# Kernel tuning notes

Hardware: AMD Instinct MI355X
Metric: run time of the kernel (lower is better)

Reference implementation:

```python
import jax, jax.numpy as jnp
import numpy as np

B, S, H, NH = 8, 4096, 1024, 16
HD = H // NH


def setup_inputs() -> dict:
    key = jax.random.key(0)
    ks = jax.random.split(key, 8)
    sd = 1.0 / np.sqrt(H)
    return {
        "hidden_states": jax.random.normal(ks[0], (B, S, H), jnp.float32),
        "attention_mask": jnp.zeros((B, 1, S), jnp.float32),
        "Wq": jax.random.normal(ks[1], (H, H), jnp.float32) * sd,
        "bq": jnp.zeros((H,), jnp.float32),
        "Wqa": jax.random.normal(ks[2], (H, NH), jnp.float32) * sd,
        "bqa": jnp.zeros((NH,), jnp.float32),
        "Wk": jax.random.normal(ks[3], (H, H), jnp.float32) * sd,
        "bk": jnp.zeros((H,), jnp.float32),
        "Wka": jax.random.normal(ks[4], (H, NH), jnp.float32) * sd,
        "bka": jnp.zeros((NH,), jnp.float32),
        "Wt": jax.random.normal(ks[5], (H, H), jnp.float32) * sd,
        "bt": jnp.zeros((H,), jnp.float32),
    }


def reference(hidden_states, attention_mask, Wq, bq, Wqa, bqa, Wk, bk, Wka, bka, Wt, bt):
    b, s, h = hidden_states.shape
    nh = Wqa.shape[1]
    hd = h // nh
    scale = 1.0 / np.sqrt(hd).astype(np.float32)

    mq = hidden_states @ Wq + bq                      # [b,s,h]
    mk = hidden_states @ Wk + bk                      # [b,s,h]

    # global query pooling
    qs = jnp.swapaxes(mq @ Wqa + bqa, 1, 2) * scale + attention_mask   # [b,nh,s]
    qw = jax.nn.softmax(qs, axis=-1)                  # [b,nh,s]
    ql = jnp.swapaxes(mq.reshape(b, s, nh, hd), 1, 2) # [b,nh,s,hd]
    pq = jnp.einsum('bns,bnsd->bnd', qw, ql).reshape(b, 1, h)  # pooled query, broadcast over seq

    # elementwise gating + global key pooling
    mqk = mk * pq                                     # [b,s,h]
    qks = jnp.swapaxes(mqk @ Wka + bka, 1, 2) * scale + attention_mask  # [b,nh,s]
    qkw = jax.nn.softmax(qks, axis=-1)                # [b,nh,s]
    kl = jnp.swapaxes(mqk.reshape(b, s, nh, hd), 1, 2)  # [b,nh,s,hd]
    pk = jnp.einsum('bns,bnsd->bnd', qkw, kl)[:, :, None, :]  # [b,nh,1,hd]

    wv = jnp.swapaxes(pk * ql, 1, 2).reshape(b, s, h) # [b,s,h]
    return wv @ Wt + bt + mq
```

## Files before the change

### kernel.cpp

```cpp
#include <hip/hip_runtime.h>
#include <hip/hip_bf16.h>
#include <stdint.h>
#include <stddef.h>

#define B_  8
#define S_  4096
#define H_  1024
#define NH_ 16
#define HD_ 64
#define PCH 32

typedef __bf16 bf16x8 __attribute__((ext_vector_type(8)));
typedef float  floatx4 __attribute__((ext_vector_type(4)));

__device__ __forceinline__ float bf2f(unsigned short u) {
    union { unsigned int i; float f; } x;
    x.i = ((unsigned int)u) << 16;
    return x.f;
}
__device__ __forceinline__ unsigned short f2bf(float f) {
    union { float f; unsigned int i; } x;
    x.f = f;
    return (unsigned short)((x.i + 0x7FFFu + ((x.i >> 16) & 1u)) >> 16);
}

__global__ __launch_bounds__(256) void k_f32_to_bf16(const float* __restrict__ src,
                                                     unsigned short* __restrict__ dst,
                                                     int n4) {
    int idx = blockIdx.x * 256 + threadIdx.x;
    if (idx >= n4) return;
    float4 v = ((const float4*)src)[idx];
    ushort4 o;
    o.x = f2bf(v.x); o.y = f2bf(v.y); o.z = f2bf(v.z); o.w = f2bf(v.w);
    ((ushort4*)dst)[idx] = o;
}

__global__ __launch_bounds__(256) void k_transpose_bf16(const float* __restrict__ w,
                                                        unsigned short* __restrict__ wt) {
    int idx = blockIdx.x * 256 + threadIdx.x;
    int k = idx >> 10, n = idx & (H_ - 1);
    wt[(n << 10) | k] = f2bf(w[idx]);
}

template <int MODE>
__global__ __launch_bounds__(256) void k_gemm_bt(const unsigned short* __restrict__ A,
                                                 const unsigned short* __restrict__ BT,
                                                 const float* __restrict__ bias,
                                                 void* __restrict__ Cout,
                                                 const unsigned short* __restrict__ addsrc,
                                                 int M, int N, int K) {
    constexpr int BM = 128, BN = 128, BK = 32, LDSW = 40;
    __shared__ unsigned short As[BM * LDSW];
    __shared__ unsigned short Bs[BN * LDSW];

    const int tid  = threadIdx.x;
    const int wave = tid >> 6, lane = tid & 63;
    const int quad = lane >> 4, m16 = lane & 15;
    const int wm = wave >> 1, wn = wave & 1;
    const int rowBase = blockIdx.y * BM;
    const int colBase = blockIdx.x * BN;

    floatx4 acc[4][4] = {};

    const int ar = tid >> 1;
    const int ac = tid & 1;
    const uint4* agp = (const uint4*)(A + (size_t)(rowBase + ar) * K + ac * 16);
    const uint4* bgp = (const uint4*)(BT + (size_t)(colBase + ar) * K + ac * 16);
    uint4* asp = (uint4*)(As + ar * LDSW + ac * 16);
    uint4* bsp = (uint4*)(Bs + ar * LDSW + ac * 16);

    for (int kt = 0; kt < K; kt += BK) {
        uint4 a0 = agp[0], a1 = agp[1];
        uint4 b0 = bgp[0], b1 = bgp[1];
        agp += BK / 8; bgp += BK / 8;
        __syncthreads();
        asp[0] = a0; asp[1] = a1;
        bsp[0] = b0; bsp[1] = b1;
        __syncthreads();
        bf16x8 af[4], bfr[4];
#pragma unroll
        for (int i = 0; i < 4; i++)
            af[i] = *(const bf16x8*)(As + (wm * 64 + i * 16 + m16) * LDSW + quad * 8);
#pragma unroll
        for (int j = 0; j < 4; j++)
            bfr[j] = *(const bf16x8*)(Bs + (wn * 64 + j * 16 + m16) * LDSW + quad * 8);
#pragma unroll
        for (int i = 0; i < 4; i++)
#pragma unroll
            for (int j = 0; j < 4; j++)
                acc[i][j] = __builtin_amdgcn_mfma_f32_16x16x32_bf16(af[i], bfr[j], acc[i][j], 0, 0, 0);
    }

#pragma unroll
    for (int i = 0; i < 4; i++) {
        const int row0 = rowBase + wm * 64 + i * 16 + quad * 4;
#pragma unroll
        for (int j = 0; j < 4; j++) {
            const int col = colBase + wn * 64 + j * 16 + m16;
            const float bv = bias[col];
#pragma unroll
            for (int r = 0; r < 4; r++) {
                const size_t off = (size_t)(row0 + r) * N + col;
                const float v = acc[i][j][r] + bv;
                if constexpr (MODE == 0) {
                    ((unsigned short*)Cout)[off] = f2bf(v);
                } else {
                    ((float*)Cout)[off] = v + bf2f(addsrc[off]);
                }
            }
        }
    }
}

__global__ __launch_bounds__(256) void k_score(const unsigned short* __restrict__ A,
                                               const float* __restrict__ W,
                                               const float* __restrict__ bias,
                                               const float* __restrict__ mask,
                                               float* __restrict__ out) {
    __shared__ float Ws[H_ * NH_];
    const int tid = threadIdx.x;
    for (int i = tid; i < H_ * NH_; i += 256) Ws[i] = W[i];
    __syncthreads();
    const int row = blockIdx.x * 16 + (tid >> 4);
    const int n = tid & 15;
    const int b = row >> 12, s = row & (S_ - 1);
    const unsigned short* arow = A + (size_t)row * H_;
    float dot = 0.f;
    for (int h = 0; h < H_; h += 8) {
        union { uint4 v; unsigned short u[8]; } x;
        x.v = *(const uint4*)(arow + h);
#pragma unroll
        for (int e = 0; e < 8; e++)
            dot += bf2f(x.u[e]) * Ws[(h + e) * NH_ + n];
    }
    out[((size_t)(b * NH_ + n)) * S_ + s] = (dot + bias[n]) * 0.125f + mask[row];
}

__global__ __launch_bounds__(256) void k_softmax(float* __restrict__ p) {
    float* row = p + (size_t)blockIdx.x * S_;
    const int tid = threadIdx.x;
    const int lane = tid & 63, wave = tid >> 6;
    __shared__ float red[4];

    float mx = -1e30f;
    for (int i = tid; i < S_; i += 256) mx = fmaxf(mx, row[i]);
#pragma unroll
    for (int off = 32; off > 0; off >>= 1) mx = fmaxf(mx, __shfl_xor(mx, off, 64));
    if (lane == 0) red[wave] = mx;
    __syncthreads();
    mx = fmaxf(fmaxf(red[0], red[1]), fmaxf(red[2], red[3]));
    __syncthreads();

    float sum = 0.f;
    for (int i = tid; i < S_; i += 256) {
        float e = __expf(row[i] - mx);
        row[i] = e;
        sum += e;
    }
#pragma unroll
    for (int off = 32; off > 0; off >>= 1) sum += __shfl_xor(sum, off, 64);
    if (lane == 0) red[wave] = sum;
    __syncthreads();
    const float inv = 1.f / (red[0] + red[1] + red[2] + red[3]);
    for (int i = tid; i < S_; i += 256) row[i] *= inv;
}

__global__ __launch_bounds__(256) void k_pool1(const float* __restrict__ w,
                                               const unsigned short* __restrict__ m,
                                               float* __restrict__ partial) {
    const int c = blockIdx.x;
    const int b = blockIdx.y >> 4;
    const int n = blockIdx.y & 15;
    const int tid = threadIdx.x;
    const int d = tid & 63, g = tid >> 6;
    const int s0 = c * (S_ / PCH);
    const float* wr = w + ((size_t)(b * NH_ + n)) * S_;
    const unsigned short* mb = m + ((size_t)b * S_) * H_ + n * HD_ + d;
    float acc = 0.f;
#pragma unroll 4
    for (int i = 0; i < S_ / PCH / 4; i++) {
        const int s = s0 + g + 4 * i;
        acc += wr[s] * bf2f(mb[(size_t)s * H_]);
    }
    __shared__ float red[4][64];
    red[g][d] = acc;
    __syncthreads();
    if (tid < 64)
        partial[((size_t)c * B_ + b) * H_ + n * HD_ + d] =
            red[0][d] + red[1][d] + red[2][d] + red[3][d];
}

__global__ __launch_bounds__(256) void k_pool2(const float* __restrict__ partial,
                                               float* __restrict__ out) {
    const int idx = blockIdx.x * 256 + threadIdx.x;
    float acc = 0.f;
#pragma unroll
    for (int c = 0; c < PCH; c++)
        acc += partial[(size_t)c * (B_ * H_) + idx];
    out[idx] = acc;
}

__global__ __launch_bounds__(256) void k_gate(const unsigned short* __restrict__ src,
                                              const float* __restrict__ scale,
                                              unsigned short* __restrict__ dst) {
    const size_t idx = ((size_t)blockIdx.x * 256 + threadIdx.x) * 8;
    const int b = (int)(idx >> 22);
    const int h = (int)(idx & (H_ - 1));
    union { uint4 v; unsigned short u[8]; } x;
    x.v = *(const uint4*)(src + idx);
    const float* sc = scale + b * H_ + h;
#pragma unroll
    for (int e = 0; e < 8; e++)
        x.u[e] = f2bf(bf2f(x.u[e]) * sc[e]);
    *(uint4*)(dst + idx) = x.v;
}

extern "C" void kernel_launch(void* const* d_in, const int* in_sizes, int n_in,
                              void* d_out, int out_size, void* d_ws, size_t ws_size,
                              hipStream_t stream) {
    (void)in_sizes; (void)n_in; (void)out_size; (void)ws_size;
    const float* hs   = (const float*)d_in[0];
    const float* mask = (const float*)d_in[1];
    const float* Wq   = (const float*)d_in[2];
    const float* bq   = (const float*)d_in[3];
    const float* Wqa  = (const float*)d_in[4];
    const float* bqa  = (const float*)d_in[5];
    const float* Wk   = (const float*)d_in[6];
    const float* bk   = (const float*)d_in[7];
    const float* Wka  = (const float*)d_in[8];
    const float* bka  = (const float*)d_in[9];
    const float* Wt   = (const float*)d_in[10];
    const float* bt   = (const float*)d_in[11];
    float* out = (float*)d_out;

    const size_t NEL = (size_t)B_ * S_ * H_;
    char* ws = (char*)d_ws;
    unsigned short* hs_bf = (unsigned short*)ws; ws += NEL * 2;
    unsigned short* mq_bf = (unsigned short*)ws; ws += NEL * 2;
    unsigned short* mk_bf = (unsigned short*)ws; ws += NEL * 2;
    unsigned short* WTq   = (unsigned short*)ws; ws += (size_t)H_ * H_ * 2;
    unsigned short* WTk   = (unsigned short*)ws; ws += (size_t)H_ * H_ * 2;
    unsigned short* WTt   = (unsigned short*)ws; ws += (size_t)H_ * H_ * 2;
    float* qs = (float*)ws; ws += (size_t)B_ * NH_ * S_ * 4;
    float* pq = (float*)ws; ws += (size_t)B_ * H_ * 4;
    float* pk = (float*)ws; ws += (size_t)B_ * H_ * 4;
    float* ppart = (float*)WTq;

    const int M = B_ * S_;
    dim3 ggrid(H_ / 128, M / 128);
    dim3 pgrid(PCH, B_ * NH_);

    k_f32_to_bf16<<<(int)(NEL / 4 / 256), 256, 0, stream>>>(hs, hs_bf, (int)(NEL / 4));
    k_transpose_bf16<<<H_ * H_ / 256, 256, 0, stream>>>(Wq, WTq);
    k_transpose_bf16<<<H_ * H_ / 256, 256, 0, stream>>>(Wk, WTk);
    k_transpose_bf16<<<H_ * H_ / 256, 256, 0, stream>>>(Wt, WTt);

    k_gemm_bt<0><<<ggrid, 256, 0, stream>>>(hs_bf, WTq, bq, mq_bf, nullptr, M, H_, H_);
    k_gemm_bt<0><<<ggrid, 256, 0, stream>>>(hs_bf, WTk, bk, mk_bf, nullptr, M, H_, H_);

    k_score<<<M / 16, 256, 0, stream>>>(mq_bf, Wqa, bqa, mask, qs);
    k_softmax<<<B_ * NH_, 256, 0, stream>>>(qs);
    k_pool1<<<pgrid, 256, 0, stream>>>(qs, mq_bf, ppart);
    k_pool2<<<B_ * H_ / 256, 256, 0, stream>>>(ppart, pq);

    k_gate<<<(int)(NEL / 8 / 256), 256, 0, stream>>>(mk_bf, pq, hs_bf);

    k_score<<<M / 16, 256, 0, stream>>>(hs_bf, Wka, bka, mask, qs);
    k_softmax<<<B_ * NH_, 256, 0, stream>>>(qs);
    k_pool1<<<pgrid, 256, 0, stream>>>(qs, hs_bf, ppart);
    k_pool2<<<B_ * H_ / 256, 256, 0, stream>>>(ppart, pk);

    k_gate<<<(int)(NEL / 8 / 256), 256, 0, stream>>>(mq_bf, pk, mk_bf);

    k_gemm_bt<1><<<ggrid, 256, 0, stream>>>(mk_bf, WTt, bt, out, mq_bf, M, H_, H_);
}
```

Measured before the change: 867.2 us.

## Load GEMM tiles directly into LDS with XOR-swizzled layout

Replaces the register-staged global-to-shared copy in the bf16 MFMA GEMM with global_load_lds direct transfers of 16 bytes per lane. It drops the padded LDS row stride and uses an XOR swizzle on the 8-element chunk index to avoid bank conflicts, with fragment offsets precomputed outside the k loop. The goal is to cut VGPR staging and LDS store instructions. The loop is still single-buffered and relies on the barrier waiting for the asynchronous LDS DMA to complete.

```diff
diff --git a/kernel.cpp b/kernel.cpp
--- a/kernel.cpp
+++ b/kernel.cpp
@@ -22,6 +22,13 @@
     union { float f; unsigned int i; } x;
     x.f = f;
     return (unsigned short)((x.i + 0x7FFFu + ((x.i >> 16) & 1u)) >> 16);
+}
+
+__device__ __forceinline__ void gl_lds16(const unsigned short* g, unsigned short* l) {
+    __builtin_amdgcn_global_load_lds(
+        (const __attribute__((address_space(1))) unsigned int*)g,
+        (__attribute__((address_space(3))) unsigned int*)l,
+        16, 0, 0);
 }
 
 __global__ __launch_bounds__(256) void k_f32_to_bf16(const float* __restrict__ src,
@@ -49,9 +56,9 @@
                                                  void* __restrict__ Cout,
                                                  const unsigned short* __restrict__ addsrc,
                                                  int M, int N, int K) {
-    constexpr int BM = 128, BN = 128, BK = 32, LDSW = 40;
-    __shared__ unsigned short As[BM * LDSW];
-    __shared__ unsigned short Bs[BN * LDSW];
+    constexpr int BM = 128, BN = 128, BK = 32;
+    __shared__ unsigned short As[BM * BK];
+    __shared__ unsigned short Bs[BN * BK];
 
     const int tid  = threadIdx.x;
     const int wave = tid >> 6, lane = tid & 63;
@@ -62,28 +69,41 @@
 
     floatx4 acc[4][4] = {};
 
-    const int ar = tid >> 1;
-    const int ac = tid & 1;
-    const uint4* agp = (const uint4*)(A + (size_t)(rowBase + ar) * K + ac * 16);
-    const uint4* bgp = (const uint4*)(BT + (size_t)(colBase + ar) * K + ac * 16);
-    uint4* asp = (uint4*)(As + ar * LDSW + ac * 16);
-    uint4* bsp = (uint4*)(Bs + ar * LDSW + ac * 16);
+    const int rl0 = 32 * wave + (lane >> 2);
+    const int rl1 = rl0 + 16;
+    const int c0 = (lane & 3) ^ ((rl0 >> 1) & 3);
+    const int c1 = (lane & 3) ^ ((rl1 >> 1) & 3);
+    const unsigned short* ga0 = A  + (size_t)(rowBase + rl0) * K + c0 * 8;
+    const unsigned short* ga1 = A  + (size_t)(rowBase + rl1) * K + c1 * 8;
+    const unsigned short* gb0 = BT + (size_t)(colBase + rl0) * K + c0 * 8;
+    const unsigned short* gb1 = BT + (size_t)(colBase + rl1) * K + c1 * 8;
+    unsigned short* la0 = As + (32 * wave) * BK;
+    unsigned short* la1 = la0 + 16 * BK;
+    unsigned short* lb0 = Bs + (32 * wave) * BK;
+    unsigned short* lb1 = lb0 + 16 * BK;
+
+    int aoff[4], boff[4];
+#pragma unroll
+    for (int i = 0; i < 4; i++) {
+        const int ra = wm * 64 + i * 16 + m16;
+        aoff[i] = ra * BK + (quad ^ ((ra >> 1) & 3)) * 8;
+        const int rb = wn * 64 + i * 16 + m16;
+        boff[i] = rb * BK + (quad ^ ((rb >> 1) & 3)) * 8;
+    }
 
     for (int kt = 0; kt < K; kt += BK) {
-        uint4 a0 = agp[0], a1 = agp[1];
-        uint4 b0 = bgp[0], b1 = bgp[1];
-        agp += BK / 8; bgp += BK / 8;
         __syncthreads();
-        asp[0] = a0; asp[1] = a1;
-        bsp[0] = b0; bsp[1] = b1;
+        gl_lds16(ga0 + kt, la0);
+        gl_lds16(ga1 + kt, la1);
+        gl_lds16(gb0 + kt, lb0);
+        gl_lds16(gb1 + kt, lb1);
         __syncthreads();
+
         bf16x8 af[4], bfr[4];
 #pragma unroll
-        for (int i = 0; i < 4; i++)
-            af[i] = *(const bf16x8*)(As + (wm * 64 + i * 16 + m16) * LDSW + quad * 8);
-#pragma unroll
-        for (int j = 0; j < 4; j++)
-            bfr[j] = *(const bf16x8*)(Bs + (wn * 64 + j * 16 + m16) * LDSW + quad * 8);
+        for (int i = 0; i < 4; i++) af[i]  = *(const bf16x8*)(As + aoff[i]);
+#pragma unroll
+        for (int j = 0; j < 4; j++) bfr[j] = *(const bf16x8*)(Bs + boff[j]);
 #pragma unroll
         for (int i = 0; i < 4; i++)
 #pragma unroll
```

Measured after the change: 841.5 us. 3.0% less time.
